# Performance work log

Measured on AMD Instinct MI355X. Metric: run time of the kernel, lower is better.

## Reference

```python
import jax, jax.numpy as jnp
import numpy as np

D = 512
P = 1024
E = 256
OUT = 500


def setup_inputs() -> dict:
    key = jax.random.key(0)
    ks = jax.random.split(key, 10)
    s = 1.0 / np.sqrt(D)
    s2 = 1.0 / np.sqrt(2 * D)
    return {
        "post": jax.random.normal(ks[0], (P, D), dtype=jnp.float32),
        "emoji": jax.random.normal(ks[1], (E, D), dtype=jnp.float32),
        "k1_w": jax.random.normal(ks[2], (D, D), dtype=jnp.float32) * s,
        "k1_b": jax.random.normal(ks[3], (D,), dtype=jnp.float32) * s,
        "k2_w": jax.random.normal(ks[4], (D, D), dtype=jnp.float32) * s,
        "k2_b": jax.random.normal(ks[5], (D,), dtype=jnp.float32) * s,
        "l1_w": jax.random.normal(ks[6], (2 * D, D), dtype=jnp.float32) * s2,
        "l1_b": jax.random.normal(ks[7], (D,), dtype=jnp.float32) * s2,
        "l2_w": jax.random.normal(ks[8], (D, OUT), dtype=jnp.float32) * s,
        "l2_b": jax.random.normal(ks[9], (D if False else OUT,), dtype=jnp.float32) * s,
    }


def reference(post, emoji, k1_w, k1_b, k2_w, k2_b, l1_w, l1_b, l2_w, l2_b):
    # k1/k2 projections: [P, D], [E, D]
    p = post @ k1_w + k1_b
    e = emoji @ k2_w + k2_b
    # l1 on concat([tile(p), tile(e)], -1) == p @ W1_post + e @ W1_emoji + b,
    # broadcast-added over the pairwise grid (same math, avoids explicit tile+cat)
    d = post.shape[1]
    pp = p @ l1_w[:d]   # [P, D]
    ee = e @ l1_w[d:]   # [E, D]
    h = jax.nn.relu(pp[:, None, :] + ee[None, :, :] + l1_b)  # [P, E, D]
    out = jax.nn.relu(h @ l2_w + l2_b)  # [P, E, OUT]
    return out
```

## Files before the change

### kernel.cpp

```cpp
#include <hip/hip_runtime.h>
#include <hip/hip_bf16.h>

#define D_DIM 512
#define P_DIM 1024
#define E_DIM 256
#define OUT_DIM 500

typedef __attribute__((ext_vector_type(8))) __bf16 bf16x8;
typedef __attribute__((ext_vector_type(4))) float f32x4;

__device__ __forceinline__ unsigned short f2bf(float f) {
    unsigned u = __builtin_bit_cast(unsigned, f);
    u += 0x7FFFu + ((u >> 16) & 1u);
    return (unsigned short)(u >> 16);
}

__device__ __forceinline__ unsigned pack2(float a, float b) {
    return (unsigned)f2bf(a) | ((unsigned)f2bf(b) << 16);
}

__global__ void cast_bf16_kernel(const float* __restrict__ in,
                                 unsigned short* __restrict__ out, int n) {
    int i = blockIdx.x * 256 + threadIdx.x;
    if (i < n) out[i] = f2bf(in[i]);
}

__global__ void transpose_cast_kernel(const float* __restrict__ in,
                                      unsigned short* __restrict__ out,
                                      int R, int C, int Cpad) {
    __shared__ float tile[32][33];
    int c0 = blockIdx.x * 32, r0 = blockIdx.y * 32;
    #pragma unroll
    for (int s = 0; s < 32; s += 8) {
        int r = r0 + threadIdx.y + s, c = c0 + threadIdx.x;
        tile[threadIdx.y + s][threadIdx.x] = (r < R && c < C) ? in[r * C + c] : 0.f;
    }
    __syncthreads();
    #pragma unroll
    for (int s = 0; s < 32; s += 8) {
        int c = c0 + threadIdx.y + s, r = r0 + threadIdx.x;
        if (c < Cpad && r < R) out[c * R + r] = f2bf(tile[threadIdx.x][threadIdx.y + s]);
    }
}

__device__ __forceinline__ void store_out(float* p, float v) { *p = v; }
__device__ __forceinline__ void store_out(unsigned short* p, float v) { *p = f2bf(v); }

template <typename OutT>
__global__ __launch_bounds__(256)
void gemm128_kernel(const unsigned short* __restrict__ A,
                    const unsigned short* __restrict__ Bt,
                    const float* __restrict__ bias,
                    OutT* __restrict__ Cd, int M, int N, int K) {
    __shared__ __align__(16) unsigned short As[128 * 40];
    __shared__ __align__(16) unsigned short Bs[128 * 40];
    const int t = threadIdx.x;
    const int m0 = blockIdx.x * 128, n0 = blockIdx.y * 128;
    const int r = t >> 1, kh = (t & 1) * 16;
    const int w = t >> 6, l = t & 63;
    const int wm = (w & 1) * 64, wn = (w >> 1) * 64;
    const int lr = l & 15, lq = l >> 4;

    f32x4 acc[4][4];
    #pragma unroll
    for (int a = 0; a < 4; a++)
        #pragma unroll
        for (int b = 0; b < 4; b++) acc[a][b] = (f32x4){0.f, 0.f, 0.f, 0.f};

    const unsigned short* aRow = &A[(m0 + r) * K];
    const unsigned short* bRow = &Bt[(n0 + r) * K];

    for (int k0 = 0; k0 < K; k0 += 32) {
        uint4 a0 = *reinterpret_cast<const uint4*>(&aRow[k0 + kh]);
        uint4 a1 = *reinterpret_cast<const uint4*>(&aRow[k0 + kh + 8]);
        uint4 b0 = *reinterpret_cast<const uint4*>(&bRow[k0 + kh]);
        uint4 b1 = *reinterpret_cast<const uint4*>(&bRow[k0 + kh + 8]);
        __syncthreads();
        *reinterpret_cast<uint4*>(&As[r * 40 + kh])     = a0;
        *reinterpret_cast<uint4*>(&As[r * 40 + kh + 8]) = a1;
        *reinterpret_cast<uint4*>(&Bs[r * 40 + kh])     = b0;
        *reinterpret_cast<uint4*>(&Bs[r * 40 + kh + 8]) = b1;
        __syncthreads();
        bf16x8 af[4], bfr[4];
        #pragma unroll
        for (int mi = 0; mi < 4; mi++)
            af[mi] = *reinterpret_cast<const bf16x8*>(&As[(wm + mi * 16 + lr) * 40 + lq * 8]);
        #pragma unroll
        for (int ni = 0; ni < 4; ni++)
            bfr[ni] = *reinterpret_cast<const bf16x8*>(&Bs[(wn + ni * 16 + lr) * 40 + lq * 8]);
        #pragma unroll
        for (int mi = 0; mi < 4; mi++)
            #pragma unroll
            for (int ni = 0; ni < 4; ni++)
                acc[mi][ni] = __builtin_amdgcn_mfma_f32_16x16x32_bf16(af[mi], bfr[ni], acc[mi][ni], 0, 0, 0);
    }

    #pragma unroll
    for (int ni = 0; ni < 4; ni++) {
        int n = n0 + wn + ni * 16 + lr;
        float bv = bias ? bias[n] : 0.f;
        #pragma unroll
        for (int mi = 0; mi < 4; mi++) {
            int m = m0 + wm + mi * 16 + lq * 4;
            #pragma unroll
            for (int rg = 0; rg < 4; rg++)
                store_out(&Cd[(m + rg) * N + n], acc[mi][ni][rg] + bv);
        }
    }
}

__global__ __launch_bounds__(256)
void pair_mlp_kernel(const float* __restrict__ pp, const float* __restrict__ ee,
                     const unsigned short* __restrict__ w2t,
                     const float* __restrict__ b2, float* __restrict__ out) {
    __shared__ __align__(16) unsigned short As[128 * 40];
    __shared__ __align__(16) unsigned short Bs[128 * 40];
    __shared__ float pps[D_DIM];

    const int t = threadIdx.x;
    const int mtile = blockIdx.x;
    const int n0 = blockIdx.y * 128;
    const int i = mtile >> 1;
    const int j0 = (mtile & 1) * 128;
    const long pairBase = (long)mtile * 128;

    const int r = t >> 1, kh = (t & 1) * 16;
    const int w = t >> 6, l = t & 63;
    const int wm = (w & 1) * 64, wn = (w >> 1) * 64;
    const int lr = l & 15, lq = l >> 4;

    pps[t] = pp[i * D_DIM + t];
    pps[t + 256] = pp[i * D_DIM + t + 256];

    f32x4 acc[4][4];
    #pragma unroll
    for (int a = 0; a < 4; a++)
        #pragma unroll
        for (int b = 0; b < 4; b++) acc[a][b] = (f32x4){0.f, 0.f, 0.f, 0.f};

    const float* eeRow = &ee[(j0 + r) * D_DIM];
    const unsigned short* wRow = &w2t[(n0 + r) * D_DIM];

    for (int k0 = 0; k0 < D_DIM; k0 += 32) {
        f32x4 ev0 = *reinterpret_cast<const f32x4*>(&eeRow[k0 + kh]);
        f32x4 ev1 = *reinterpret_cast<const f32x4*>(&eeRow[k0 + kh + 4]);
        f32x4 ev2 = *reinterpret_cast<const f32x4*>(&eeRow[k0 + kh + 8]);
        f32x4 ev3 = *reinterpret_cast<const f32x4*>(&eeRow[k0 + kh + 12]);
        uint4 wv0 = *reinterpret_cast<const uint4*>(&wRow[k0 + kh]);
        uint4 wv1 = *reinterpret_cast<const uint4*>(&wRow[k0 + kh + 8]);
        __syncthreads();
        f32x4 pv0 = *reinterpret_cast<const f32x4*>(&pps[k0 + kh]);
        f32x4 pv1 = *reinterpret_cast<const f32x4*>(&pps[k0 + kh + 4]);
        f32x4 pv2 = *reinterpret_cast<const f32x4*>(&pps[k0 + kh + 8]);
        f32x4 pv3 = *reinterpret_cast<const f32x4*>(&pps[k0 + kh + 12]);
        f32x4 s0 = pv0 + ev0, s1 = pv1 + ev1, s2 = pv2 + ev2, s3 = pv3 + ev3;
        #pragma unroll
        for (int x = 0; x < 4; x++) {
            s0[x] = s0[x] > 0.f ? s0[x] : 0.f;
            s1[x] = s1[x] > 0.f ? s1[x] : 0.f;
            s2[x] = s2[x] > 0.f ? s2[x] : 0.f;
            s3[x] = s3[x] > 0.f ? s3[x] : 0.f;
        }
        uint4 h0, h1;
        h0.x = pack2(s0[0], s0[1]); h0.y = pack2(s0[2], s0[3]);
        h0.z = pack2(s1[0], s1[1]); h0.w = pack2(s1[2], s1[3]);
        h1.x = pack2(s2[0], s2[1]); h1.y = pack2(s2[2], s2[3]);
        h1.z = pack2(s3[0], s3[1]); h1.w = pack2(s3[2], s3[3]);
        *reinterpret_cast<uint4*>(&As[r * 40 + kh])     = h0;
        *reinterpret_cast<uint4*>(&As[r * 40 + kh + 8]) = h1;
        *reinterpret_cast<uint4*>(&Bs[r * 40 + kh])     = wv0;
        *reinterpret_cast<uint4*>(&Bs[r * 40 + kh + 8]) = wv1;
        __syncthreads();
        bf16x8 af[4], bfr[4];
        #pragma unroll
        for (int mi = 0; mi < 4; mi++)
            af[mi] = *reinterpret_cast<const bf16x8*>(&As[(wm + mi * 16 + lr) * 40 + lq * 8]);
        #pragma unroll
        for (int ni = 0; ni < 4; ni++)
            bfr[ni] = *reinterpret_cast<const bf16x8*>(&Bs[(wn + ni * 16 + lr) * 40 + lq * 8]);
        #pragma unroll
        for (int mi = 0; mi < 4; mi++)
            #pragma unroll
            for (int ni = 0; ni < 4; ni++)
                acc[mi][ni] = __builtin_amdgcn_mfma_f32_16x16x32_bf16(af[mi], bfr[ni], acc[mi][ni], 0, 0, 0);
    }

    #pragma unroll
    for (int ni = 0; ni < 4; ni++) {
        int n = n0 + wn + ni * 16 + lr;
        bool valid = n < OUT_DIM;
        float bv = valid ? b2[n] : 0.f;
        #pragma unroll
        for (int mi = 0; mi < 4; mi++) {
            int row = wm + mi * 16 + lq * 4;
            float* op = &out[(pairBase + row) * OUT_DIM + n];
            if (valid) {
                #pragma unroll
                for (int rg = 0; rg < 4; rg++) {
                    float v = acc[mi][ni][rg] + bv;
                    op[(long)rg * OUT_DIM] = v > 0.f ? v : 0.f;
                }
            }
        }
    }
}

extern "C" void kernel_launch(void* const* d_in, const int* in_sizes, int n_in,
                              void* d_out, int out_size, void* d_ws, size_t ws_size,
                              hipStream_t stream) {
    const float* post  = (const float*)d_in[0];
    const float* emoji = (const float*)d_in[1];
    const float* k1_w  = (const float*)d_in[2];
    const float* k1_b  = (const float*)d_in[3];
    const float* k2_w  = (const float*)d_in[4];
    const float* k2_b  = (const float*)d_in[5];
    const float* l1_w  = (const float*)d_in[6];
    const float* l1_b  = (const float*)d_in[7];
    const float* l2_w  = (const float*)d_in[8];
    const float* l2_b  = (const float*)d_in[9];
    float* out = (float*)d_out;

    char* wp = (char*)d_ws;
    auto alloc = [&](size_t bytes) { char* q = wp; wp += (bytes + 255) & ~(size_t)255; return q; };
    unsigned short* post_bf  = (unsigned short*)alloc(P_DIM * D_DIM * 2);
    unsigned short* emoji_bf = (unsigned short*)alloc(E_DIM * D_DIM * 2);
    unsigned short* k1_wt    = (unsigned short*)alloc(D_DIM * D_DIM * 2);
    unsigned short* k2_wt    = (unsigned short*)alloc(D_DIM * D_DIM * 2);
    unsigned short* l1at     = (unsigned short*)alloc(D_DIM * D_DIM * 2);
    unsigned short* l1bt     = (unsigned short*)alloc(D_DIM * D_DIM * 2);
    unsigned short* w2t      = (unsigned short*)alloc(512 * 512 * 2);
    unsigned short* p_bf     = (unsigned short*)alloc(P_DIM * D_DIM * 2);
    unsigned short* e_bf     = (unsigned short*)alloc(E_DIM * D_DIM * 2);
    float* pp  = (float*)alloc(P_DIM * D_DIM * 4);
    float* eeb = (float*)alloc(E_DIM * D_DIM * 4);

    cast_bf16_kernel<<<P_DIM * D_DIM / 256, 256, 0, stream>>>(post, post_bf, P_DIM * D_DIM);
    cast_bf16_kernel<<<E_DIM * D_DIM / 256, 256, 0, stream>>>(emoji, emoji_bf, E_DIM * D_DIM);

    dim3 tb(32, 8);
    transpose_cast_kernel<<<dim3(16, 16), tb, 0, stream>>>(k1_w, k1_wt, 512, 512, 512);
    transpose_cast_kernel<<<dim3(16, 16), tb, 0, stream>>>(k2_w, k2_wt, 512, 512, 512);
    transpose_cast_kernel<<<dim3(16, 16), tb, 0, stream>>>(l1_w, l1at, 512, 512, 512);
    transpose_cast_kernel<<<dim3(16, 16), tb, 0, stream>>>(l1_w + 512 * 512, l1bt, 512, 512, 512);
    transpose_cast_kernel<<<dim3(16, 16), tb, 0, stream>>>(l2_w, w2t, 512, 500, 512);

    gemm128_kernel<unsigned short><<<dim3(8, 4), 256, 0, stream>>>(post_bf, k1_wt, k1_b, p_bf, 1024, 512, 512);
    gemm128_kernel<unsigned short><<<dim3(2, 4), 256, 0, stream>>>(emoji_bf, k2_wt, k2_b, e_bf, 256, 512, 512);
    gemm128_kernel<float><<<dim3(8, 4), 256, 0, stream>>>(p_bf, l1at, (const float*)nullptr, pp, 1024, 512, 512);
    gemm128_kernel<float><<<dim3(2, 4), 256, 0, stream>>>(e_bf, l1bt, l1_b, eeb, 256, 512, 512);

    pair_mlp_kernel<<<dim3(2048, 4), 256, 0, stream>>>(pp, eeb, w2t, l2_b, out);
}
```

Measured before the change: 883.9 us.

## Fold weight products, merge prep launches, widen pair MLP tile to 256 columns

```diff
diff --git a/kernel.cpp b/kernel.cpp
--- a/kernel.cpp
+++ b/kernel.cpp
@@ -5,6 +5,7 @@
 #define P_DIM 1024
 #define E_DIM 256
 #define OUT_DIM 500
+#define STR 36
 
 typedef __attribute__((ext_vector_type(8))) __bf16 bf16x8;
 typedef __attribute__((ext_vector_type(4))) float f32x4;
@@ -14,48 +15,146 @@
     u += 0x7FFFu + ((u >> 16) & 1u);
     return (unsigned short)(u >> 16);
 }
-
 __device__ __forceinline__ unsigned pack2(float a, float b) {
     return (unsigned)f2bf(a) | ((unsigned)f2bf(b) << 16);
 }
 
-__global__ void cast_bf16_kernel(const float* __restrict__ in,
-                                 unsigned short* __restrict__ out, int n) {
-    int i = blockIdx.x * 256 + threadIdx.x;
-    if (i < n) out[i] = f2bf(in[i]);
-}
-
-__global__ void transpose_cast_kernel(const float* __restrict__ in,
-                                      unsigned short* __restrict__ out,
-                                      int R, int C, int Cpad) {
-    __shared__ float tile[32][33];
-    int c0 = blockIdx.x * 32, r0 = blockIdx.y * 32;
-    #pragma unroll
-    for (int s = 0; s < 32; s += 8) {
-        int r = r0 + threadIdx.y + s, c = c0 + threadIdx.x;
-        tile[threadIdx.y + s][threadIdx.x] = (r < R && c < C) ? in[r * C + c] : 0.f;
-    }
-    __syncthreads();
-    #pragma unroll
-    for (int s = 0; s < 32; s += 8) {
-        int c = c0 + threadIdx.y + s, r = r0 + threadIdx.x;
-        if (c < Cpad && r < R) out[c * R + r] = f2bf(tile[threadIdx.x][threadIdx.y + s]);
-    }
-}
-
-__device__ __forceinline__ void store_out(float* p, float v) { *p = v; }
-__device__ __forceinline__ void store_out(unsigned short* p, float v) { *p = f2bf(v); }
-
-template <typename OutT>
 __global__ __launch_bounds__(256)
-void gemm128_kernel(const unsigned short* __restrict__ A,
-                    const unsigned short* __restrict__ Bt,
-                    const float* __restrict__ bias,
-                    OutT* __restrict__ Cd, int M, int N, int K) {
-    __shared__ __align__(16) unsigned short As[128 * 40];
-    __shared__ __align__(16) unsigned short Bs[128 * 40];
+void prep_kernel(const float* __restrict__ post, const float* __restrict__ emoji,
+                 const float* __restrict__ k1_w, const float* __restrict__ k1_b,
+                 const float* __restrict__ k2_w, const float* __restrict__ k2_b,
+                 const float* __restrict__ l1_w, const float* __restrict__ l1_b,
+                 const float* __restrict__ l2_w,
+                 unsigned short* __restrict__ post_bf, unsigned short* __restrict__ emoji_bf,
+                 unsigned short* __restrict__ w2t,
+                 unsigned short* __restrict__ Wp_t, unsigned short* __restrict__ We_t,
+                 float* __restrict__ bp, float* __restrict__ be) {
+    __shared__ __align__(16) unsigned short sA[128 * STR];
+    __shared__ __align__(16) unsigned short sB[128 * STR];
+    __shared__ float ttile[32][33];
+    const int bid = blockIdx.x;
     const int t = threadIdx.x;
-    const int m0 = blockIdx.x * 128, n0 = blockIdx.y * 128;
+
+    if (bid < 32) {
+        const int mat = bid >> 4;
+        const int tileId = bid & 15;
+        const int n0 = (tileId >> 2) * 128, kk0 = (tileId & 3) * 128;
+        const float* srcA = l1_w + (size_t)mat * 512 * 512;
+        const float* srcB = mat ? k2_w : k1_w;
+        unsigned short* dst = mat ? We_t : Wp_t;
+
+        const int w = t >> 6, l = t & 63;
+        const int wm = (w & 1) * 64, wn = (w >> 1) * 64;
+        const int lr = l & 15, lq = l >> 4;
+        const int ja = t >> 3, nc = (t & 7) * 16;
+        const int rb = t >> 1, jh = (t & 1) * 16;
+
+        f32x4 acc[4][4];
+        #pragma unroll
+        for (int a = 0; a < 4; a++)
+            #pragma unroll
+            for (int b = 0; b < 4; b++) acc[a][b] = (f32x4){0.f, 0.f, 0.f, 0.f};
+
+        for (int jb = 0; jb < 512; jb += 32) {
+            f32x4 av[4], bv[4];
+            #pragma unroll
+            for (int x = 0; x < 4; x++)
+                av[x] = *reinterpret_cast<const f32x4*>(&srcA[(jb + ja) * 512 + n0 + nc + x * 4]);
+            #pragma unroll
+            for (int x = 0; x < 4; x++)
+                bv[x] = *reinterpret_cast<const f32x4*>(&srcB[(kk0 + rb) * 512 + jb + jh + x * 4]);
+            __syncthreads();
+            #pragma unroll
+            for (int x = 0; x < 4; x++)
+                #pragma unroll
+                for (int y = 0; y < 4; y++)
+                    sA[(nc + x * 4 + y) * STR + ja] = f2bf(av[x][y]);
+            uint4 bw0, bw1;
+            bw0.x = pack2(bv[0][0], bv[0][1]); bw0.y = pack2(bv[0][2], bv[0][3]);
+            bw0.z = pack2(bv[1][0], bv[1][1]); bw0.w = pack2(bv[1][2], bv[1][3]);
+            bw1.x = pack2(bv[2][0], bv[2][1]); bw1.y = pack2(bv[2][2], bv[2][3]);
+            bw1.z = pack2(bv[3][0], bv[3][1]); bw1.w = pack2(bv[3][2], bv[3][3]);
+            *reinterpret_cast<uint4*>(&sB[rb * STR + jh]) = bw0;
+            *reinterpret_cast<uint4*>(&sB[rb * STR + jh + 8]) = bw1;
+            __syncthreads();
+            bf16x8 af[4], bfr[4];
+            #pragma unroll
+            for (int mi = 0; mi < 4; mi++)
+                af[mi] = *reinterpret_cast<const bf16x8*>(&sA[(wm + mi * 16 + lr) * STR + lq * 8]);
+            #pragma unroll
+            for (int ni = 0; ni < 4; ni++)
+                bfr[ni] = *reinterpret_cast<const bf16x8*>(&sB[(wn + ni * 16 + lr) * STR + lq * 8]);
+            #pragma unroll
+            for (int mi = 0; mi < 4; mi++)
+                #pragma unroll
+                for (int ni = 0; ni < 4; ni++)
+                    acc[mi][ni] = __builtin_amdgcn_mfma_f32_16x16x32_bf16(af[mi], bfr[ni], acc[mi][ni], 0, 0, 0);
+        }
+        #pragma unroll
+        for (int ni = 0; ni < 4; ni++) {
+            int k = kk0 + wn + ni * 16 + lr;
+            #pragma unroll
+            for (int mi = 0; mi < 4; mi++) {
+                int n = n0 + wm + mi * 16 + lq * 4;
+                #pragma unroll
+                for (int rg = 0; rg < 4; rg++)
+                    dst[(n + rg) * 512 + k] = f2bf(acc[mi][ni][rg]);
+            }
+        }
+    } else if (bid < 34) {
+        const int which = bid - 32;
+        const float* kb = which ? k2_b : k1_b;
+        const float* lw = l1_w + (size_t)which * 512 * 512;
+        float a0 = 0.f, a1 = 0.f;
+        for (int k = 0; k < 512; k++) {
+            float s = kb[k];
+            a0 += s * lw[k * 512 + t];
+            a1 += s * lw[k * 512 + t + 256];
+        }
+        if (which) { a0 += l1_b[t]; a1 += l1_b[t + 256]; }
+        float* dst = which ? be : bp;
+        dst[t] = a0; dst[t + 256] = a1;
+    } else if (bid < 290) {
+        const int wb = bid - 34;
+        const int c0 = (wb & 15) * 32, r0 = (wb >> 4) * 32;
+        const int tx = t & 31, ty = t >> 5;
+        #pragma unroll
+        for (int s = 0; s < 32; s += 8) {
+            int r = r0 + ty + s, c = c0 + tx;
+            ttile[ty + s][tx] = (c < OUT_DIM) ? l2_w[r * OUT_DIM + c] : 0.f;
+        }
+        __syncthreads();
+        #pragma unroll
+        for (int s = 0; s < 32; s += 8) {
+            int c = c0 + ty + s, r = r0 + tx;
+            w2t[c * 512 + r] = f2bf(ttile[tx][ty + s]);
+        }
+    } else if (bid < 546) {
+        const int cb = bid - 290;
+        const int idx = cb * 2048 + t * 8;
+        f32x4 v0 = *reinterpret_cast<const f32x4*>(&post[idx]);
+        f32x4 v1 = *reinterpret_cast<const f32x4*>(&post[idx + 4]);
+        uint4 o;
+        o.x = pack2(v0[0], v0[1]); o.y = pack2(v0[2], v0[3]);
+        o.z = pack2(v1[0], v1[1]); o.w = pack2(v1[2], v1[3]);
+        *reinterpret_cast<uint4*>(&post_bf[idx]) = o;
+    } else {
+        const int cb = bid - 546;
+        const int idx = cb * 2048 + t * 8;
+        f32x4 v0 = *reinterpret_cast<const f32x4*>(&emoji[idx]);
+        f32x4 v1 = *reinterpret_cast<const f32x4*>(&emoji[idx + 4]);
+        uint4 o;
+        o.x = pack2(v0[0], v0[1]); o.y = pack2(v0[2], v0[3]);
+        o.z = pack2(v1[0], v1[1]); o.w = pack2(v1[2], v1[3]);
+        *reinterpret_cast<uint4*>(&emoji_bf[idx]) = o;
+    }
+}
+
+__device__ __forceinline__
+void gemm128_body(const unsigned short* __restrict__ A, const unsigned short* __restrict__ Bt,
+                  const float* __restrict__ bias, float* __restrict__ Cd,
+                  int m0, int n0, unsigned short* sA, unsigned short* sB) {
+    const int t = threadIdx.x;
     const int r = t >> 1, kh = (t & 1) * 16;
     const int w = t >> 6, l = t & 63;
     const int wm = (w & 1) * 64, wn = (w >> 1) * 64;
@@ -67,134 +166,146 @@
         #pragma unroll
         for (int b = 0; b < 4; b++) acc[a][b] = (f32x4){0.f, 0.f, 0.f, 0.f};
 
-    const unsigned short* aRow = &A[(m0 + r) * K];
-    const unsigned short* bRow = &Bt[(n0 + r) * K];
-
-    for (int k0 = 0; k0 < K; k0 += 32) {
+    const unsigned short* aRow = &A[(m0 + r) * 512];
+    const unsigned short* bRow = &Bt[(n0 + r) * 512];
+
+    for (int k0 = 0; k0 < 512; k0 += 32) {
         uint4 a0 = *reinterpret_cast<const uint4*>(&aRow[k0 + kh]);
         uint4 a1 = *reinterpret_cast<const uint4*>(&aRow[k0 + kh + 8]);
         uint4 b0 = *reinterpret_cast<const uint4*>(&bRow[k0 + kh]);
         uint4 b1 = *reinterpret_cast<const uint4*>(&bRow[k0 + kh + 8]);
         __syncthreads();
-        *reinterpret_cast<uint4*>(&As[r * 40 + kh])     = a0;
-        *reinterpret_cast<uint4*>(&As[r * 40 + kh + 8]) = a1;
-        *reinterpret_cast<uint4*>(&Bs[r * 40 + kh])     = b0;
-        *reinterpret_cast<uint4*>(&Bs[r * 40 + kh + 8]) = b1;
+        *reinterpret_cast<uint4*>(&sA[r * STR + kh])     = a0;
+        *reinterpret_cast<uint4*>(&sA[r * STR + kh + 8]) = a1;
+        *reinterpret_cast<uint4*>(&sB[r * STR + kh])     = b0;
+        *reinterpret_cast<uint4*>(&sB[r * STR + kh + 8]) = b1;
         __syncthreads();
         bf16x8 af[4], bfr[4];
         #pragma unroll
         for (int mi = 0; mi < 4; mi++)
-            af[mi] = *reinterpret_cast<const bf16x8*>(&As[(wm + mi * 16 + lr) * 40 + lq * 8]);
+            af[mi] = *reinterpret_cast<const bf16x8*>(&sA[(wm + mi * 16 + lr) * STR + lq * 8]);
         #pragma unroll
         for (int ni = 0; ni < 4; ni++)
-            bfr[ni] = *reinterpret_cast<const bf16x8*>(&Bs[(wn + ni * 16 + lr) * 40 + lq * 8]);
+            bfr[ni] = *reinterpret_cast<const bf16x8*>(&sB[(wn + ni * 16 + lr) * STR + lq * 8]);
         #pragma unroll
         for (int mi = 0; mi < 4; mi++)
             #pragma unroll
             for (int ni = 0; ni < 4; ni++)
                 acc[mi][ni] = __builtin_amdgcn_mfma_f32_16x16x32_bf16(af[mi], bfr[ni], acc[mi][ni], 0, 0, 0);
     }
-
     #pragma unroll
     for (int ni = 0; ni < 4; ni++) {
         int n = n0 + wn + ni * 16 + lr;
-        float bv = bias ? bias[n] : 0.f;
+        float bv = bias[n];
         #pragma unroll
         for (int mi = 0; mi < 4; mi++) {
             int m = m0 + wm + mi * 16 + lq * 4;
             #pragma unroll
             for (int rg = 0; rg < 4; rg++)
-                store_out(&Cd[(m + rg) * N + n], acc[mi][ni][rg] + bv);
+                Cd[(m + rg) * 512 + n] = acc[mi][ni][rg] + bv;
         }
     }
 }
 
 __global__ __launch_bounds__(256)
+void proj_kernel(const unsigned short* __restrict__ post_bf, const unsigned short* __restrict__ emoji_bf,
+                 const unsigned short* __restrict__ Wp_t, const unsigned short* __restrict__ We_t,
+                 const float* __restrict__ bp, const float* __restrict__ be,
+                 float* __restrict__ pp, float* __restrict__ eeb) {
+    __shared__ __align__(16) unsigned short sA[128 * STR];
+    __shared__ __align__(16) unsigned short sB[128 * STR];
+    const int bid = blockIdx.x;
+    if (bid < 32)
+        gemm128_body(post_bf, Wp_t, bp, pp, (bid >> 2) * 128, (bid & 3) * 128, sA, sB);
+    else {
+        int b2i = bid - 32;
+        gemm128_body(emoji_bf, We_t, be, eeb, (b2i >> 2) * 128, (b2i & 3) * 128, sA, sB);
+    }
+}
+
+__global__ __launch_bounds__(256, 2)
 void pair_mlp_kernel(const float* __restrict__ pp, const float* __restrict__ ee,
                      const unsigned short* __restrict__ w2t,
                      const float* __restrict__ b2, float* __restrict__ out) {
-    __shared__ __align__(16) unsigned short As[128 * 40];
-    __shared__ __align__(16) unsigned short Bs[128 * 40];
+    __shared__ __align__(16) unsigned short As[128 * STR];
+    __shared__ __align__(16) unsigned short Bs[256 * STR];
     __shared__ float pps[D_DIM];
 
     const int t = threadIdx.x;
     const int mtile = blockIdx.x;
-    const int n0 = blockIdx.y * 128;
-    const int i = mtile >> 1;
-    const int j0 = (mtile & 1) * 128;
+    const int i = mtile >> 1, j0 = (mtile & 1) * 128;
+    const int n0 = blockIdx.y * 256;
     const long pairBase = (long)mtile * 128;
 
-    const int r = t >> 1, kh = (t & 1) * 16;
     const int w = t >> 6, l = t & 63;
-    const int wm = (w & 1) * 64, wn = (w >> 1) * 64;
+    const int wm = (w & 1) * 64, wn = (w >> 1) * 128;
     const int lr = l & 15, lq = l >> 4;
+    const int srow = t >> 2, sc = t & 3;
 
     pps[t] = pp[i * D_DIM + t];
-    pps[t + 256] = pp[i * D_DIM + t + 256];
-
-    f32x4 acc[4][4];
+    pps[t + 256] = pp[i * D_DIM + 256 + t];
+
+    f32x4 acc[4][8];
     #pragma unroll
     for (int a = 0; a < 4; a++)
         #pragma unroll
-        for (int b = 0; b < 4; b++) acc[a][b] = (f32x4){0.f, 0.f, 0.f, 0.f};
-
-    const float* eeRow = &ee[(j0 + r) * D_DIM];
-    const unsigned short* wRow = &w2t[(n0 + r) * D_DIM];
+        for (int b = 0; b < 8; b++) acc[a][b] = (f32x4){0.f, 0.f, 0.f, 0.f};
 
     for (int k0 = 0; k0 < D_DIM; k0 += 32) {
-        f32x4 ev0 = *reinterpret_cast<const f32x4*>(&eeRow[k0 + kh]);
-        f32x4 ev1 = *reinterpret_cast<const f32x4*>(&eeRow[k0 + kh + 4]);
-        f32x4 ev2 = *reinterpret_cast<const f32x4*>(&eeRow[k0 + kh + 8]);
-        f32x4 ev3 = *reinterpret_cast<const f32x4*>(&eeRow[k0 + kh + 12]);
-        uint4 wv0 = *reinterpret_cast<const uint4*>(&wRow[k0 + kh]);
-        uint4 wv1 = *reinterpret_cast<const uint4*>(&wRow[k0 + kh + 8]);
-        __syncthreads();
-        f32x4 pv0 = *reinterpret_cast<const f32x4*>(&pps[k0 + kh]);
-        f32x4 pv1 = *reinterpret_cast<const f32x4*>(&pps[k0 + kh + 4]);
-        f32x4 pv2 = *reinterpret_cast<const f32x4*>(&pps[k0 + kh + 8]);
-        f32x4 pv3 = *reinterpret_cast<const f32x4*>(&pps[k0 + kh + 12]);
-        f32x4 s0 = pv0 + ev0, s1 = pv1 + ev1, s2 = pv2 + ev2, s3 = pv3 + ev3;
-        #pragma unroll
-        for (int x = 0; x < 4; x++) {
-            s0[x] = s0[x] > 0.f ? s0[x] : 0.f;
-            s1[x] = s1[x] > 0.f ? s1[x] : 0.f;
-            s2[x] = s2[x] > 0.f ? s2[x] : 0.f;
-            s3[x] = s3[x] > 0.f ? s3[x] : 0.f;
-        }
-        uint4 h0, h1;
-        h0.x = pack2(s0[0], s0[1]); h0.y = pack2(s0[2], s0[3]);
-        h0.z = pack2(s1[0], s1[1]); h0.w = pack2(s1[2], s1[3]);
-        h1.x = pack2(s2[0], s2[1]); h1.y = pack2(s2[2], s2[3]);
-        h1.z = pack2(s3[0], s3[1]); h1.w = pack2(s3[2], s3[3]);
-        *reinterpret_cast<uint4*>(&As[r * 40 + kh])     = h0;
-        *reinterpret_cast<uint4*>(&As[r * 40 + kh + 8]) = h1;
-        *reinterpret_cast<uint4*>(&Bs[r * 40 + kh])     = wv0;
-        *reinterpret_cast<uint4*>(&Bs[r * 40 + kh + 8]) = wv1;
-        __syncthreads();
-        bf16x8 af[4], bfr[4];
+        f32x4 ea[2], eb[2];
+        uint4 wv[4];
+        #pragma unroll
+        for (int rp = 0; rp < 2; rp++) {
+            const float* src = &ee[(j0 + rp * 64 + srow) * D_DIM + k0 + sc * 8];
+            ea[rp] = *reinterpret_cast<const f32x4*>(src);
+            eb[rp] = *reinterpret_cast<const f32x4*>(src + 4);
+        }
+        #pragma unroll
+        for (int rp = 0; rp < 4; rp++)
+            wv[rp] = *reinterpret_cast<const uint4*>(&w2t[(n0 + rp * 64 + srow) * 512 + k0 + sc * 8]);
+        __syncthreads();
+        f32x4 p0 = *reinterpret_cast<const f32x4*>(&pps[k0 + sc * 8]);
+        f32x4 p1 = *reinterpret_cast<const f32x4*>(&pps[k0 + sc * 8 + 4]);
+        #pragma unroll
+        for (int rp = 0; rp < 2; rp++) {
+            f32x4 s0 = ea[rp] + p0, s1 = eb[rp] + p1;
+            #pragma unroll
+            for (int x = 0; x < 4; x++) {
+                s0[x] = s0[x] > 0.f ? s0[x] : 0.f;
+                s1[x] = s1[x] > 0.f ? s1[x] : 0.f;
+            }
+            uint4 h;
+            h.x = pack2(s0[0], s0[1]); h.y = pack2(s0[2], s0[3]);
+            h.z = pack2(s1[0], s1[1]); h.w = pack2(s1[2], s1[3]);
+            *reinterpret_cast<uint4*>(&As[(rp * 64 + srow) * STR + sc * 8]) = h;
+        }
+        #pragma unroll
+        for (int rp = 0; rp < 4; rp++)
+            *reinterpret_cast<uint4*>(&Bs[(rp * 64 + srow) * STR + sc * 8]) = wv[rp];
+        __syncthreads();
+        bf16x8 af[4], bfr[8];
         #pragma unroll
         for (int mi = 0; mi < 4; mi++)
-            af[mi] = *reinterpret_cast<const bf16x8*>(&As[(wm + mi * 16 + lr) * 40 + lq * 8]);
-        #pragma unroll
-        for (int ni = 0; ni < 4; ni++)
-            bfr[ni] = *reinterpret_cast<const bf16x8*>(&Bs[(wn + ni * 16 + lr) * 40 + lq * 8]);
+            af[mi] = *reinterpret_cast<const bf16x8*>(&As[(wm + mi * 16 + lr) * STR + lq * 8]);
+        #pragma unroll
+        for (int ni = 0; ni < 8; ni++)
+            bfr[ni] = *reinterpret_cast<const bf16x8*>(&Bs[(wn + ni * 16 + lr) * STR + lq * 8]);
         #pragma unroll
         for (int mi = 0; mi < 4; mi++)
             #pragma unroll
-            for (int ni = 0; ni < 4; ni++)
+            for (int ni = 0; ni < 8; ni++)
                 acc[mi][ni] = __builtin_amdgcn_mfma_f32_16x16x32_bf16(af[mi], bfr[ni], acc[mi][ni], 0, 0, 0);
     }
 
     #pragma unroll
-    for (int ni = 0; ni < 4; ni++) {
+    for (int ni = 0; ni < 8; ni++) {
         int n = n0 + wn + ni * 16 + lr;
-        bool valid = n < OUT_DIM;
-        float bv = valid ? b2[n] : 0.f;
-        #pragma unroll
-        for (int mi = 0; mi < 4; mi++) {
-            int row = wm + mi * 16 + lq * 4;
-            float* op = &out[(pairBase + row) * OUT_DIM + n];
-            if (valid) {
+        if (n < OUT_DIM) {
+            float bv = b2[n];
+            #pragma unroll
+            for (int mi = 0; mi < 4; mi++) {
+                int m = wm + mi * 16 + lq * 4;
+                float* op = &out[(pairBase + m) * OUT_DIM + n];
                 #pragma unroll
                 for (int rg = 0; rg < 4; rg++) {
                     float v = acc[mi][ni][rg] + bv;
@@ -224,30 +335,16 @@
     auto alloc = [&](size_t bytes) { char* q = wp; wp += (bytes + 255) & ~(size_t)255; return q; };
     unsigned short* post_bf  = (unsigned short*)alloc(P_DIM * D_DIM * 2);
     unsigned short* emoji_bf = (unsigned short*)alloc(E_DIM * D_DIM * 2);
-    unsigned short* k1_wt    = (unsigned short*)alloc(D_DIM * D_DIM * 2);
-    unsigned short* k2_wt    = (unsigned short*)alloc(D_DIM * D_DIM * 2);
-    unsigned short* l1at     = (unsigned short*)alloc(D_DIM * D_DIM * 2);
-    unsigned short* l1bt     = (unsigned short*)alloc(D_DIM * D_DIM * 2);
     unsigned short* w2t      = (unsigned short*)alloc(512 * 512 * 2);
-    unsigned short* p_bf     = (unsigned short*)alloc(P_DIM * D_DIM * 2);
-    unsigned short* e_bf     = (unsigned short*)alloc(E_DIM * D_DIM * 2);
+    unsigned short* Wp_t     = (unsigned short*)alloc(512 * 512 * 2);
+    unsigned short* We_t     = (unsigned short*)alloc(512 * 512 * 2);
+    float* bp  = (float*)alloc(512 * 4);
+    float* be  = (float*)alloc(512 * 4);
     float* pp  = (float*)alloc(P_DIM * D_DIM * 4);
     float* eeb = (float*)alloc(E_DIM * D_DIM * 4);
 
-    cast_bf16_kernel<<<P_DIM * D_DIM / 256, 256, 0, stream>>>(post, post_bf, P_DIM * D_DIM);
-    cast_bf16_kernel<<<E_DIM * D_DIM / 256, 256, 0, stream>>>(emoji, emoji_bf, E_DIM * D_DIM);
-
-    dim3 tb(32, 8);
-    transpose_cast_kernel<<<dim3(16, 16), tb, 0, stream>>>(k1_w, k1_wt, 512, 512, 512);
-    transpose_cast_kernel<<<dim3(16, 16), tb, 0, stream>>>(k2_w, k2_wt, 512, 512, 512);
-    transpose_cast_kernel<<<dim3(16, 16), tb, 0, stream>>>(l1_w, l1at, 512, 512, 512);
-    transpose_cast_kernel<<<dim3(16, 16), tb, 0, stream>>>(l1_w + 512 * 512, l1bt, 512, 512, 512);
-    transpose_cast_kernel<<<dim3(16, 16), tb, 0, stream>>>(l2_w, w2t, 512, 500, 512);
-
-    gemm128_kernel<unsigned short><<<dim3(8, 4), 256, 0, stream>>>(post_bf, k1_wt, k1_b, p_bf, 1024, 512, 512);
-    gemm128_kernel<unsigned short><<<dim3(2, 4), 256, 0, stream>>>(emoji_bf, k2_wt, k2_b, e_bf, 256, 512, 512);
-    gemm128_kernel<float><<<dim3(8, 4), 256, 0, stream>>>(p_bf, l1at, (const float*)nullptr, pp, 1024, 512, 512);
-    gemm128_kernel<float><<<dim3(2, 4), 256, 0, stream>>>(e_bf, l1bt, l1_b, eeb, 256, 512, 512);
-
-    pair_mlp_kernel<<<dim3(2048, 4), 256, 0, stream>>>(pp, eeb, w2t, l2_b, out);
-}
+    prep_kernel<<<610, 256, 0, stream>>>(post, emoji, k1_w, k1_b, k2_w, k2_b, l1_w, l1_b, l2_w,
+                                         post_bf, emoji_bf, w2t, Wp_t, We_t, bp, be);
+    proj_kernel<<<40, 256, 0, stream>>>(post_bf, emoji_bf, Wp_t, We_t, bp, be, pp, eeb);
+    pair_mlp_kernel<<<dim3(2048, 2), 256, 0, stream>>>(pp, eeb, w2t, l2_b, out);
+}
```

Result: slower. 978.8 us (+10.7%).
